# Optimization experiments

Hardware: AMD Instinct MI355X
Metric: run time of the kernel (lower is better)

The kernel has to match this reference:

```python
import jax, jax.numpy as jnp
import numpy as np


def setup_inputs() -> dict:
    key = jax.random.key(0)
    k1, k2 = jax.random.split(key)
    B, C = 8192, 50257
    # probabilities must be strictly positive since the module takes log directly
    pred = jax.random.uniform(k1, (B, C), dtype=jnp.float32, minval=1e-6, maxval=1.0)
    label = jax.random.randint(k2, (B,), 0, C, dtype=jnp.int64)
    return {"pred": pred, "label": label}


def reference(pred, label):
    # mean over batch of -log(pred[i, label[i]])  (fused gather-log-reduce)
    picked = jnp.take_along_axis(pred, label[:, None], axis=1)[:, 0]  # [B]
    return -jnp.mean(jnp.log(picked))
```

## Files before the change

### kernel.cpp

```cpp
#include <hip/hip_runtime.h>
#include <hip/hip_bf16.h>


__global__ __launch_bounds__(1024)
void ce_gather_log_mean(const float* __restrict__ pred,
                        const int* __restrict__ label,
                        float* __restrict__ out,
                        int B, long long C) {
    const int tid = threadIdx.x;
    float acc = 0.0f;

    #pragma unroll 8
    for (int i = tid; i < B; i += 1024) {
        int lbl = label[i];
        float p = pred[(long long)i * C + (long long)lbl];
        acc += logf(p);
    }

    #pragma unroll
    for (int off = 32; off > 0; off >>= 1)
        acc += __shfl_down(acc, off, 64);

    __shared__ float s_partial[16];
    const int wave = tid >> 6;
    const int lane = tid & 63;
    if (lane == 0) s_partial[wave] = acc;
    __syncthreads();

    if (tid == 0) {
        float total = 0.0f;
        #pragma unroll
        for (int w = 0; w < 16; ++w) total += s_partial[w];
        out[0] = -total / (float)B;
    }
}

extern "C" void kernel_launch(void* const* d_in, const int* in_sizes, int n_in,
                              void* d_out, int out_size, void* d_ws, size_t ws_size,
                              hipStream_t stream) {
    const float* pred  = (const float*)d_in[0];
    const int*   label = (const int*)d_in[1];
    float*       out   = (float*)d_out;

    const int B = in_sizes[1];
    const long long C = (long long)in_sizes[0] / (long long)B;

    ce_gather_log_mean<<<1, 1024, 0, stream>>>(pred, label, out, B, C);
}
```

Measured before the change: 10.40 us.

## Spread gather-log reduction across many 64-thread blocks with atomic accumulation

Replaces the single 1024-thread block, which looped over all rows, with one wavefront-sized block per 64 rows. Each block reduces its rows with shuffles and atomically adds its scaled partial sum to the output, which is zeroed by a memset first. The goal is to spread the latency-bound scattered loads across many compute units instead of one. In exchange it adds a memset launch and 128 float atomics, which makes the summation order nondeterministic.

```diff
diff --git a/kernel.cpp b/kernel.cpp
--- a/kernel.cpp
+++ b/kernel.cpp
@@ -2,37 +2,25 @@
 #include <hip/hip_bf16.h>
 
 
-__global__ __launch_bounds__(1024)
+__global__ __launch_bounds__(64)
 void ce_gather_log_mean(const float* __restrict__ pred,
                         const int* __restrict__ label,
                         float* __restrict__ out,
                         int B, long long C) {
-    const int tid = threadIdx.x;
-    float acc = 0.0f;
+    const int i = blockIdx.x * 64 + threadIdx.x;
 
-    #pragma unroll 8
-    for (int i = tid; i < B; i += 1024) {
-        int lbl = label[i];
-        float p = pred[(long long)i * C + (long long)lbl];
-        acc += logf(p);
+    float v = 0.0f;
+    if (i < B) {
+        const int lbl = label[i];
+        v = logf(pred[(long long)i * C + (long long)lbl]);
     }
 
     #pragma unroll
     for (int off = 32; off > 0; off >>= 1)
-        acc += __shfl_down(acc, off, 64);
+        v += __shfl_down(v, off, 64);
 
-    __shared__ float s_partial[16];
-    const int wave = tid >> 6;
-    const int lane = tid & 63;
-    if (lane == 0) s_partial[wave] = acc;
-    __syncthreads();
-
-    if (tid == 0) {
-        float total = 0.0f;
-        #pragma unroll
-        for (int w = 0; w < 16; ++w) total += s_partial[w];
-        out[0] = -total / (float)B;
-    }
+    if (threadIdx.x == 0)
+        atomicAdd(out, -v / (float)B);
 }
 
 extern "C" void kernel_launch(void* const* d_in, const int* in_sizes, int n_in,
@@ -45,5 +33,8 @@
     const int B = in_sizes[1];
     const long long C = (long long)in_sizes[0] / (long long)B;
 
-    ce_gather_log_mean<<<1, 1024, 0, stream>>>(pred, label, out, B, C);
+    hipMemsetAsync(out, 0, sizeof(float), stream);
+
+    const int blocks = (B + 63) / 64;
+    ce_gather_log_mean<<<blocks, 64, 0, stream>>>(pred, label, out, B, C);
 }
```

Measured after the change: 12.57 us. 1.21x slower.
